# Optimization experiments

Measured on AMD Instinct MI355X. Metric: run time of the kernel, lower is better.

Reference implementation:

```python
import jax, jax.numpy as jnp
import numpy as np

MARGIN = 1.0


def setup_inputs() -> dict:
    key = jax.random.key(0)
    k1, k2, k3 = jax.random.split(key, 3)
    B, P = 8192, 16
    return {
        "energies": jax.random.normal(k1, (B, 1), dtype=jnp.float32),
        "property_values": jax.random.normal(k2, (B, P), dtype=jnp.float32),
        "property_targets": jax.random.normal(k3, (P,), dtype=jnp.float32),
    }


def reference(energies, property_values, property_targets):
    # distances[i] = ||property_values[i] - property_targets||_2, shape [B]
    distances = jnp.linalg.norm(property_values - property_targets[None, :], axis=-1)
    B = energies.shape[0]
    e = energies[:, 0]  # [B]
    # pair mask: i != j and distances[i] < distances[j]  -> [B, B]
    mask = (distances[:, None] < distances[None, :]) & (~jnp.eye(B, dtype=bool))
    # ranking loss per pair: relu(e_i - e_j + margin)
    pair_loss = jax.nn.relu(e[:, None] - e[None, :] + MARGIN)
    loss_sum = jnp.sum(jnp.where(mask, pair_loss, 0.0))
    count = jnp.sum(mask).astype(jnp.float32)
    loss = loss_sum / jnp.maximum(count, 1.0)
    # torch version accumulates [1]-shaped tensors -> output shape [1]
    return loss[None]
```

## Files before the change

kernel.cpp:

```cpp
#include <hip/hip_runtime.h>
#include <math.h>

#define MARGIN 1.0f
#define TI 256
#define TJ 512

__global__ __launch_bounds__(256) void dist_kernel(
    const float* __restrict__ pv,
    const float* __restrict__ pt,
    float* __restrict__ dist,
    int B, int P)
{
    int i = blockIdx.x * blockDim.x + threadIdx.x;
    if (i >= B) return;
    const float* row = pv + (size_t)i * P;
    float s = 0.f;
    for (int p = 0; p < P; ++p) {
        float d = row[p] - pt[p];
        s = fmaf(d, d, s);
    }
    dist[i] = sqrtf(s);
}

__global__ __launch_bounds__(256) void pair_kernel(
    const float* __restrict__ e,
    const float* __restrict__ dist,
    float* __restrict__ psum,
    float* __restrict__ pcnt,
    int B, int nj_tiles)
{
    __shared__ float sd[TJ];
    __shared__ float se[TJ];

    int it = blockIdx.x / nj_tiles;
    int jt = blockIdx.x % nj_tiles;
    int j0 = jt * TJ;

    for (int k = threadIdx.x; k < TJ; k += 256) {
        int j = j0 + k;
        bool ok = (j < B);
        sd[k] = ok ? dist[j] : -INFINITY;
        se[k] = ok ? e[j]    : 0.f;
    }
    __syncthreads();

    int i = it * TI + (int)threadIdx.x;
    bool iok = (i < B);
    float di = iok ? dist[i] : INFINITY;
    float a  = iok ? (e[i] + MARGIN) : 0.f;

    float sum = 0.f, cnt = 0.f;
    #pragma unroll 8
    for (int k = 0; k < TJ; ++k) {
        float dj = sd[k];
        float ej = se[k];
        bool m  = (di < dj);
        float t = fmaxf(a - ej, 0.f);
        sum += m ? t   : 0.f;
        cnt += m ? 1.f : 0.f;
    }

    __shared__ float rs[256];
    __shared__ float rc[256];
    rs[threadIdx.x] = sum;
    rc[threadIdx.x] = cnt;
    __syncthreads();
    for (int s = 128; s > 0; s >>= 1) {
        if ((int)threadIdx.x < s) {
            rs[threadIdx.x] += rs[threadIdx.x + s];
            rc[threadIdx.x] += rc[threadIdx.x + s];
        }
        __syncthreads();
    }
    if (threadIdx.x == 0) {
        psum[blockIdx.x] = rs[0];
        pcnt[blockIdx.x] = rc[0];
    }
}

__global__ __launch_bounds__(256) void finalize_kernel(
    const float* __restrict__ psum,
    const float* __restrict__ pcnt,
    float* __restrict__ out,
    int nblk)
{
    __shared__ double ss[256];
    __shared__ double sc[256];
    double s = 0.0, c = 0.0;
    for (int k = threadIdx.x; k < nblk; k += 256) {
        s += (double)psum[k];
        c += (double)pcnt[k];
    }
    ss[threadIdx.x] = s;
    sc[threadIdx.x] = c;
    __syncthreads();
    for (int st = 128; st > 0; st >>= 1) {
        if ((int)threadIdx.x < st) {
            ss[threadIdx.x] += ss[threadIdx.x + st];
            sc[threadIdx.x] += sc[threadIdx.x + st];
        }
        __syncthreads();
    }
    if (threadIdx.x == 0) {
        double cnt = sc[0] < 1.0 ? 1.0 : sc[0];
        out[0] = (float)(ss[0] / cnt);
    }
}

extern "C" void kernel_launch(void* const* d_in, const int* in_sizes, int n_in,
                              void* d_out, int out_size, void* d_ws, size_t ws_size,
                              hipStream_t stream)
{
    const float* energies = (const float*)d_in[0];
    const float* pv       = (const float*)d_in[1];
    const float* pt       = (const float*)d_in[2];
    int B = in_sizes[0];
    int P = in_sizes[2];

    int ni = (B + TI - 1) / TI;
    int nj = (B + TJ - 1) / TJ;
    int nblk = ni * nj;

    float* dist = (float*)d_ws;
    float* psum = dist + B;
    float* pcnt = psum + nblk;

    dist_kernel<<<(B + 255) / 256, 256, 0, stream>>>(pv, pt, dist, B, P);
    pair_kernel<<<nblk, 256, 0, stream>>>(energies, dist, psum, pcnt, B, nj);
    finalize_kernel<<<1, 256, 0, stream>>>(psum, pcnt, (float*)d_out, nblk);
}
```

Measured before the change: 75.17 us.

## Fuse pair reduction with atomic finalize and register-block 16 rows per thread

Each block now stages all distances and energies in shared memory. Each thread keeps 16 i-values in registers and sweeps j across the full array. Counts come from wavefront ballot/popcount, and the sums go through a wave shuffle reduction. Block partials are added with double atomics, and a last-block ticket writes the final loss, which removes the separate finalize launch. The distance kernel is vectorised with float4 and also resets the control block. The change assumes B <= 8192 and B divisible by 4, and it uses 64KB of LDS per block, which limits occupancy.

```diff
diff --git a/kernel.cpp b/kernel.cpp
--- a/kernel.cpp
+++ b/kernel.cpp
@@ -2,108 +2,115 @@
 #include <math.h>
 
 #define MARGIN 1.0f
-#define TI 256
-#define TJ 512
+#define NI 16
+#define BMAX 8192
 
-__global__ __launch_bounds__(256) void dist_kernel(
+struct Ctl {
+    double sacc;
+    double cacc;
+    unsigned ticket;
+    unsigned pad;
+};
+
+__global__ __launch_bounds__(256) void dist_init_kernel(
     const float* __restrict__ pv,
     const float* __restrict__ pt,
     float* __restrict__ dist,
+    Ctl* __restrict__ ctl,
     int B, int P)
 {
-    int i = blockIdx.x * blockDim.x + threadIdx.x;
+    int i = blockIdx.x * 256 + threadIdx.x;
+    if (i == 0) { ctl->sacc = 0.0; ctl->cacc = 0.0; ctl->ticket = 0u; }
     if (i >= B) return;
     const float* row = pv + (size_t)i * P;
     float s = 0.f;
-    for (int p = 0; p < P; ++p) {
-        float d = row[p] - pt[p];
-        s = fmaf(d, d, s);
+    if (P == 16) {
+        const float4* r4 = (const float4*)row;
+        const float4* t4 = (const float4*)pt;
+        #pragma unroll
+        for (int q = 0; q < 4; ++q) {
+            float4 r = r4[q], t = t4[q];
+            float d0 = r.x - t.x; s = fmaf(d0, d0, s);
+            float d1 = r.y - t.y; s = fmaf(d1, d1, s);
+            float d2 = r.z - t.z; s = fmaf(d2, d2, s);
+            float d3 = r.w - t.w; s = fmaf(d3, d3, s);
+        }
+    } else {
+        for (int p = 0; p < P; ++p) { float d = row[p] - pt[p]; s = fmaf(d, d, s); }
     }
     dist[i] = sqrtf(s);
 }
 
-__global__ __launch_bounds__(256) void pair_kernel(
+__global__ __launch_bounds__(256) void pair_fused_kernel(
     const float* __restrict__ e,
     const float* __restrict__ dist,
-    float* __restrict__ psum,
-    float* __restrict__ pcnt,
-    int B, int nj_tiles)
+    Ctl* __restrict__ ctl,
+    float* __restrict__ out,
+    int B, int nblocks)
 {
-    __shared__ float sd[TJ];
-    __shared__ float se[TJ];
+    __shared__ float sd[BMAX];
+    __shared__ float se[BMAX];
+    const int tid = threadIdx.x;
 
-    int it = blockIdx.x / nj_tiles;
-    int jt = blockIdx.x % nj_tiles;
-    int j0 = jt * TJ;
-
-    for (int k = threadIdx.x; k < TJ; k += 256) {
-        int j = j0 + k;
-        bool ok = (j < B);
-        sd[k] = ok ? dist[j] : -INFINITY;
-        se[k] = ok ? e[j]    : 0.f;
+    {
+        const float4* d4 = (const float4*)dist;
+        const float4* e4 = (const float4*)e;
+        float4* sd4 = (float4*)sd;
+        float4* se4 = (float4*)se;
+        const int n4 = B >> 2;
+        for (int k = tid; k < n4; k += 256) { sd4[k] = d4[k]; se4[k] = e4[k]; }
+        for (int k = B + tid; k < BMAX; k += 256) { sd[k] = -INFINITY; se[k] = 0.f; }
     }
     __syncthreads();
 
-    int i = it * TI + (int)threadIdx.x;
-    bool iok = (i < B);
-    float di = iok ? dist[i] : INFINITY;
-    float a  = iok ? (e[i] + MARGIN) : 0.f;
-
-    float sum = 0.f, cnt = 0.f;
-    #pragma unroll 8
-    for (int k = 0; k < TJ; ++k) {
-        float dj = sd[k];
-        float ej = se[k];
-        bool m  = (di < dj);
-        float t = fmaxf(a - ej, 0.f);
-        sum += m ? t   : 0.f;
-        cnt += m ? 1.f : 0.f;
+    const int i0 = blockIdx.x * NI;
+    float di[NI], ai[NI];
+    #pragma unroll
+    for (int ii = 0; ii < NI; ++ii) {
+        const bool iok = (i0 + ii) < B;
+        di[ii] = iok ? sd[i0 + ii] : INFINITY;
+        ai[ii] = iok ? (se[i0 + ii] + MARGIN) : 0.f;
     }
 
-    __shared__ float rs[256];
-    __shared__ float rc[256];
-    rs[threadIdx.x] = sum;
-    rc[threadIdx.x] = cnt;
+    float sv[4] = {0.f, 0.f, 0.f, 0.f};
+    unsigned cntw = 0;
+
+    #pragma unroll 2
+    for (int s = 0; s < (BMAX / 256); ++s) {
+        const int j = tid + (s << 8);
+        const float dj = sd[j];
+        const float ej = se[j];
+        #pragma unroll
+        for (int ii = 0; ii < NI; ++ii) {
+            const bool m = di[ii] < dj;
+            const float t = fmaxf(ai[ii] - ej, 0.f);
+            sv[ii & 3] += m ? t : 0.f;
+            cntw += (unsigned)__popcll(__ballot(m));
+        }
+    }
+
+    float sum = (sv[0] + sv[1]) + (sv[2] + sv[3]);
+    #pragma unroll
+    for (int o = 32; o > 0; o >>= 1) sum += __shfl_xor(sum, o);
+
     __syncthreads();
-    for (int s = 128; s > 0; s >>= 1) {
-        if ((int)threadIdx.x < s) {
-            rs[threadIdx.x] += rs[threadIdx.x + s];
-            rc[threadIdx.x] += rc[threadIdx.x + s];
+    const int wid = tid >> 6;
+    if ((tid & 63) == 0) { sd[wid] = sum; se[wid] = (float)cntw; }
+    __syncthreads();
+
+    if (tid == 0) {
+        double S = ((double)sd[0] + (double)sd[1]) + ((double)sd[2] + (double)sd[3]);
+        double C = ((double)se[0] + (double)se[1]) + ((double)se[2] + (double)se[3]);
+        atomicAdd(&ctl->sacc, S);
+        atomicAdd(&ctl->cacc, C);
+        __threadfence();
+        unsigned t = atomicAdd(&ctl->ticket, 1u);
+        if (t == (unsigned)(nblocks - 1)) {
+            double fs = atomicAdd(&ctl->sacc, 0.0);
+            double fc = atomicAdd(&ctl->cacc, 0.0);
+            if (fc < 1.0) fc = 1.0;
+            out[0] = (float)(fs / fc);
         }
-        __syncthreads();
-    }
-    if (threadIdx.x == 0) {
-        psum[blockIdx.x] = rs[0];
-        pcnt[blockIdx.x] = rc[0];
-    }
-}
-
-__global__ __launch_bounds__(256) void finalize_kernel(
-    const float* __restrict__ psum,
-    const float* __restrict__ pcnt,
-    float* __restrict__ out,
-    int nblk)
-{
-    __shared__ double ss[256];
-    __shared__ double sc[256];
-    double s = 0.0, c = 0.0;
-    for (int k = threadIdx.x; k < nblk; k += 256) {
-        s += (double)psum[k];
-        c += (double)pcnt[k];
-    }
-    ss[threadIdx.x] = s;
-    sc[threadIdx.x] = c;
-    __syncthreads();
-    for (int st = 128; st > 0; st >>= 1) {
-        if ((int)threadIdx.x < st) {
-            ss[threadIdx.x] += ss[threadIdx.x + st];
-            sc[threadIdx.x] += sc[threadIdx.x + st];
-        }
-        __syncthreads();
-    }
-    if (threadIdx.x == 0) {
-        double cnt = sc[0] < 1.0 ? 1.0 : sc[0];
-        out[0] = (float)(ss[0] / cnt);
     }
 }
 
@@ -117,15 +124,12 @@
     int B = in_sizes[0];
     int P = in_sizes[2];
 
-    int ni = (B + TI - 1) / TI;
-    int nj = (B + TJ - 1) / TJ;
-    int nblk = ni * nj;
+    float* dist = (float*)d_ws;
+    size_t coff = (((size_t)BMAX * sizeof(float)) + 255) & ~(size_t)255;
+    Ctl* ctl = (Ctl*)((char*)d_ws + coff);
 
-    float* dist = (float*)d_ws;
-    float* psum = dist + B;
-    float* pcnt = psum + nblk;
+    int nblocks = (B + NI - 1) / NI;
 
-    dist_kernel<<<(B + 255) / 256, 256, 0, stream>>>(pv, pt, dist, B, P);
-    pair_kernel<<<nblk, 256, 0, stream>>>(energies, dist, psum, pcnt, B, nj);
-    finalize_kernel<<<1, 256, 0, stream>>>(psum, pcnt, (float*)d_out, nblk);
+    dist_init_kernel<<<(B + 255) / 256, 256, 0, stream>>>(pv, pt, dist, ctl, B, P);
+    pair_fused_kernel<<<nblocks, 256, 0, stream>>>(energies, dist, ctl, (float*)d_out, B, nblocks);
 }
```

New measurement: 87.48 us. +16.4%, slower.
